# Kernel tuning notes

Hardware: AMD Instinct MI355X
Metric: run time of the kernel (lower is better)

Reference implementation:

```python
import jax, jax.numpy as jnp
import numpy as np

DIM = 768
NUM_HEADS = 12
POLY_DEG = 3
GRID = (24, 24)
BATCH = 16


def _make_powers():
    H, W = GRID
    ii, jj = np.meshgrid(np.arange(H), np.arange(W), indexing='ij')
    coords = np.stack([ii.ravel(), jj.ravel()], axis=-1).astype(np.float32)  # [HW, 2]
    dists = np.abs(coords[:, None, :] - coords[None, :, :]).sum(-1)  # L1 cdist [HW, HW]
    powers = np.stack([dists ** i for i in range(POLY_DEG + 1)], axis=0)  # [deg+1, HW, HW]
    return jnp.asarray(powers, dtype=jnp.float32)


def setup_inputs() -> dict:
    key = jax.random.key(0)
    ks = jax.random.split(key, 5)
    N = GRID[0] * GRID[1] + 1  # 577
    x = jax.random.normal(ks[0], (BATCH, N, DIM), dtype=jnp.float32)
    # nn.Linear weights stored as [in, out] for direct matmul; qkv_bias=False
    W_qkv = jax.random.normal(ks[1], (DIM, 3 * DIM), dtype=jnp.float32) * (DIM ** -0.5)
    W_proj = jax.random.normal(ks[2], (DIM, DIM), dtype=jnp.float32) * (DIM ** -0.5)
    b_proj = jnp.zeros((DIM,), dtype=jnp.float32)
    # small scale keeps polynomial bias (distances up to 46, cubed) numerically sane
    poly_coeffs = jax.random.normal(ks[3], (NUM_HEADS, POLY_DEG + 1), dtype=jnp.float32) * 0.01
    powers = _make_powers()
    return {"x": x, "W_qkv": W_qkv, "W_proj": W_proj, "b_proj": b_proj,
            "poly_coeffs": poly_coeffs, "powers": powers}


def reference(x, W_qkv, W_proj, b_proj, poly_coeffs, powers):
    B, N, C = x.shape
    h = NUM_HEADS
    d = C // h
    scale = d ** -0.5
    qkv = (x @ W_qkv).reshape(B, N, 3, h, d)
    qkv = jnp.transpose(qkv, (2, 0, 3, 1, 4))  # [3, B, h, N, d]
    q, k, v = qkv[0], qkv[1], qkv[2]
    # polynomial relative-position bias, padded with zeros for CLS row/col
    rpe = jnp.einsum('hd,dxy->hxy', poly_coeffs, powers)  # [h, HW, HW]
    rpe = jnp.pad(rpe, ((0, 0), (1, 0), (1, 0)))  # [h, N, N]
    attn = scale * jnp.einsum('bhnd,bhmd->bhnm', q, k) + rpe[None]
    attn = jax.nn.softmax(attn, axis=-1)
    out = jnp.einsum('bhnm,bhmd->bhnd', attn, v)
    out = jnp.transpose(out, (0, 2, 1, 3)).reshape(B, N, C)
    return out @ W_proj + b_proj
```

## Files before the change

kernel.cpp:

```cpp
#include <hip/hip_runtime.h>


using u16 = unsigned short;
using u32 = unsigned int;

typedef __bf16 bf16x8 __attribute__((ext_vector_type(8)));
typedef float f32x4 __attribute__((ext_vector_type(4)));

__device__ inline u16 f2bf(float f) {
    u32 u = __builtin_bit_cast(u32, f);
    u32 r = u + 0x7fffu + ((u >> 16) & 1u);
    return (u16)(r >> 16);
}
__device__ inline float bf2f(u16 x) {
    return __builtin_bit_cast(float, (u32)x << 16);
}

__device__ inline f32x4 mfma16(bf16x8 a, bf16x8 b, f32x4 c) {
    return __builtin_amdgcn_mfma_f32_16x16x32_bf16(a, b, c, 0, 0, 0);
}

__device__ inline float fexp2(float x) { return __builtin_amdgcn_exp2f(x); }

__device__ inline float dpp_max16(float v) {
    int x;
    x = __builtin_amdgcn_update_dpp(0, __builtin_bit_cast(int, v), 0xB1, 0xF, 0xF, true);
    v = fmaxf(v, __builtin_bit_cast(float, x));
    x = __builtin_amdgcn_update_dpp(0, __builtin_bit_cast(int, v), 0x4E, 0xF, 0xF, true);
    v = fmaxf(v, __builtin_bit_cast(float, x));
    x = __builtin_amdgcn_update_dpp(0, __builtin_bit_cast(int, v), 0x124, 0xF, 0xF, true);
    v = fmaxf(v, __builtin_bit_cast(float, x));
    x = __builtin_amdgcn_update_dpp(0, __builtin_bit_cast(int, v), 0x128, 0xF, 0xF, true);
    v = fmaxf(v, __builtin_bit_cast(float, x));
    return v;
}
__device__ inline float dpp_sum16(float v) {
    int x;
    x = __builtin_amdgcn_update_dpp(0, __builtin_bit_cast(int, v), 0xB1, 0xF, 0xF, true);
    v += __builtin_bit_cast(float, x);
    x = __builtin_amdgcn_update_dpp(0, __builtin_bit_cast(int, v), 0x4E, 0xF, 0xF, true);
    v += __builtin_bit_cast(float, x);
    x = __builtin_amdgcn_update_dpp(0, __builtin_bit_cast(int, v), 0x124, 0xF, 0xF, true);
    v += __builtin_bit_cast(float, x);
    x = __builtin_amdgcn_update_dpp(0, __builtin_bit_cast(int, v), 0x128, 0xF, 0xF, true);
    v += __builtin_bit_cast(float, x);
    return v;
}

#define GLOAD_LDS16(g, l)                                                          \
    __builtin_amdgcn_global_load_lds((const __attribute__((address_space(1))) u32*)(g), \
                                     (__attribute__((address_space(3))) u32*)(l), 16, 0, 0)

#define BAR()    asm volatile("s_barrier" ::: "memory")
#define WAITV4() asm volatile("s_waitcnt vmcnt(4)" ::: "memory")
#define WAITV0() asm volatile("s_waitcnt vmcnt(0)" ::: "memory")

__global__ void k_prep(const float* __restrict__ x, const float* __restrict__ Wq,
                       const float* __restrict__ Wp, u16* __restrict__ xb,
                       u16* __restrict__ wqkv, u16* __restrict__ wprj) {
    const int tid0 = blockIdx.x * blockDim.x + threadIdx.x;
    const int stride = gridDim.x * blockDim.x;
    const int n4 = 9232 * 768 / 4;
    for (int i = tid0; i < n4; i += stride) {
        float4 v = ((const float4*)x)[i];
        ushort4 o;
        o.x = f2bf(v.x); o.y = f2bf(v.y); o.z = f2bf(v.z); o.w = f2bf(v.w);
        ((ushort4*)xb)[i] = o;
    }
    for (int i = tid0; i < 768 * 2304; i += stride) {
        int r = i / 2304, c = i - r * 2304;
        wqkv[(size_t)c * 768 + r] = f2bf(Wq[i]);
    }
    for (int i = tid0; i < 768 * 768; i += stride) {
        int r = i / 768, c = i - r * 768;
        wprj[(size_t)c * 768 + r] = f2bf(Wp[i]);
    }
}

__device__ inline void stageAB(const u16* __restrict__ Ag, const u16* __restrict__ Bg,
                               u16* La, u16* Lb, int t, int w) {
#pragma unroll
    for (int c = 0; c < 2; ++c) {
        const int p = c * 256 + t;
        const int row = p >> 2, ch = p & 3;
        const int src = row * 768 + ((ch ^ ((row >> 1) & 3)) * 8);
        GLOAD_LDS16(Ag + src, La + (size_t)(c * 256 + w * 64) * 8);
        GLOAD_LDS16(Bg + src, Lb + (size_t)(c * 256 + w * 64) * 8);
    }
}
__device__ inline bf16x8 ldfrag32(const u16* base, int row, int slot) {
    return *(const bf16x8*)(base + row * 32 + ((slot ^ ((row >> 1) & 3)) * 8));
}

template <int MODE>
__launch_bounds__(256, 3)
__global__ void k_gemm(const u16* __restrict__ A, const u16* __restrict__ Bw,
                       u16* __restrict__ q_out, u16* __restrict__ k_out,
                       u16* __restrict__ v_out,
                       float* __restrict__ f_out, const float* __restrict__ bias) {
    constexpr int NT = 24;
    constexpr int M = 9232;
    const int mbase = blockIdx.y * 128;
    const int nbase = blockIdx.x * 128;
    __shared__ alignas(16) u16 lds[3][2][128 * 32];
    const int t = threadIdx.x;
    const int lane = t & 63, w = t >> 6;
    const int lr = lane & 15, lg = lane >> 4;
    const int wrow = (w >> 1) * 64, wcol = (w & 1) * 64;
    const u16* Ag = A + (size_t)mbase * 768;
    const u16* Bg = Bw + (size_t)nbase * 768;
    f32x4 acc[4][4] = {};

    stageAB(Ag, Bg, &lds[0][0][0], &lds[0][1][0], t, w);
    stageAB(Ag + 32, Bg + 32, &lds[1][0][0], &lds[1][1][0], t, w);
    WAITV4();
    BAR();

    for (int kt = 0; kt < NT; ++kt) {
        const int cb = kt % 3;
        const u16* Ab = &lds[cb][0][0];
        const u16* Bb = &lds[cb][1][0];
        const bool m2 = (kt + 2) < NT;
        if (m2) {
            const int nb = (kt + 2) % 3;
            stageAB(Ag + (kt + 2) * 32, Bg + (kt + 2) * 32,
                    &lds[nb][0][0], &lds[nb][1][0], t, w);
        }
        bf16x8 af[4], bv[4];
#pragma unroll
        for (int i = 0; i < 4; ++i)
            af[i] = ldfrag32(Ab, wrow + i * 16 + lr, lg);
#pragma unroll
        for (int j = 0; j < 4; ++j)
            bv[j] = ldfrag32(Bb, wcol + j * 16 + lr, lg);
        __builtin_amdgcn_s_setprio(1);
#pragma unroll
        for (int i = 0; i < 4; ++i)
#pragma unroll
            for (int j = 0; j < 4; ++j)
                acc[i][j] = mfma16(af[i], bv[j], acc[i][j]);
        __builtin_amdgcn_s_setprio(0);
        if (kt + 1 < NT) {
            if (m2) { WAITV4(); } else { WAITV0(); }
            BAR();
        }
    }

#pragma unroll
    for (int i = 0; i < 4; ++i) {
#pragma unroll
        for (int j = 0; j < 4; ++j) {
            const int col = nbase + wcol + j * 16 + lr;
#pragma unroll
            for (int r = 0; r < 4; ++r) {
                const int row = mbase + wrow + i * 16 + 4 * lg + r;
                if (row < M) {
                    if (MODE == 0) {
                        const int bb = row / 577;
                        const int nn = row - bb * 577;
                        const int tt = col / 768;
                        const int rem = col - tt * 768;
                        const int hh = rem >> 6, dd = rem & 63;
                        const size_t bh = (size_t)bb * 12 + hh;
                        const u16 val = f2bf(acc[i][j][r]);
                        if (tt == 0)      q_out[(bh * 640 + nn) * 64 + dd] = val;
                        else if (tt == 1) k_out[(bh * 640 + nn) * 64 + dd] = val;
                        else              v_out[(bh * 64 + dd) * 640 + nn] = val;
                    } else {
                        f_out[(size_t)row * 768 + col] = acc[i][j][r] + bias[col];
                    }
                }
            }
        }
    }
}

__launch_bounds__(256, 3)
__global__ void k_attn(const u16* __restrict__ Qg, const u16* __restrict__ Kg,
                       const u16* __restrict__ Vtg, const float* __restrict__ coef,
                       u16* __restrict__ Og) {
    const int bh = blockIdx.x;
    const int qt = blockIdx.y;
    const int b = bh / 12, h = bh - b * 12;
    const int t = threadIdx.x;
    const int lane = t & 63, w = t >> 6;
    const int lr = lane & 15, lg = lane >> 4;
    __shared__ alignas(16) u16 Kl[2][4096];
    __shared__ alignas(16) u16 Vl[2][4096];
    __shared__ alignas(16) u16 Plds[4][16 * 72];
    __shared__ float lut[256];

    {
        const float l2e = 1.4426950408889634f;
        const float c0 = coef[h * 4 + 0] * l2e, c1 = coef[h * 4 + 1] * l2e,
                    c2 = coef[h * 4 + 2] * l2e, c3 = coef[h * 4 + 3] * l2e;
        const float d = (float)t;
        lut[t] = (t <= 46) ? (((c3 * d + c2) * d + c1) * d + c0) : 0.f;
    }

    const int qrow0 = qt * 64 + w * 16;
    const u16* qp = Qg + ((size_t)bh * 640 + qrow0 + lr) * 64;
    const bf16x8 qa0 = *(const bf16x8*)(qp + lg * 8);
    const bf16x8 qa1 = *(const bf16x8*)(qp + 32 + lg * 8);

    float gi[4], gj[4];
#pragma unroll
    for (int r = 0; r < 4; ++r) {
        const int n = qrow0 + 4 * lg + r;
        if (n == 0) { gi[r] = 100.f; gj[r] = 0.f; }
        else {
            const int nm1 = n - 1;
            const int qi = nm1 / 24;
            gi[r] = (float)qi;
            gj[r] = (float)(nm1 - qi * 24);
        }
    }

    float M[4], L[4];
#pragma unroll
    for (int r = 0; r < 4; ++r) { M[r] = -3e38f; L[r] = 0.f; }
    f32x4 acco[4] = {};
    const float scale2 = 0.125f * 1.4426950408889634f;
    const int ch0 = ((lg ^ (lr & 7))) * 8;

    const u16* Ksb = Kg + (size_t)bh * 640 * 64;
    const u16* Vsb = Vtg + (size_t)bh * 64 * 640;
    const int pr0 = t >> 3, pc0 = t & 7;
    const int pr1 = (256 + t) >> 3, pc1 = (256 + t) & 7;
    const int kd0 = pr0 * 64 + ((pc0 ^ (pr0 & 7)) * 8);
    const int kd1 = pr1 * 64 + ((pc1 ^ (pr1 & 7)) * 8);

    {
        uint4 k0 = *(const uint4*)(Ksb + pr0 * 64 + pc0 * 8);
        uint4 k1 = *(const uint4*)(Ksb + pr1 * 64 + pc1 * 8);
        uint4 v0 = *(const uint4*)(Vsb + (size_t)pr0 * 640 + pc0 * 8);
        uint4 v1 = *(const uint4*)(Vsb + (size_t)pr1 * 640 + pc1 * 8);
        *(uint4*)(&Kl[0][kd0]) = k0;
        *(uint4*)(&Kl[0][kd1]) = k1;
        *(uint4*)(&Vl[0][kd0]) = v0;
        *(uint4*)(&Vl[0][kd1]) = v1;
    }
    __syncthreads();
    int cur = 0;

    for (int kt = 0; kt < 10; ++kt) {
        const bool full = (kt < 9);
        uint4 nk0, nk1, nv0, nv1;
        if (full) {
            const u16* Ks = Ksb + (size_t)(kt + 1) * 64 * 64;
            const u16* Vs = Vsb + (size_t)(kt + 1) * 64;
            nk0 = *(const uint4*)(Ks + pr0 * 64 + pc0 * 8);
            nk1 = *(const uint4*)(Ks + pr1 * 64 + pc1 * 8);
            nv0 = *(const uint4*)(Vs + (size_t)pr0 * 640 + pc0 * 8);
            nv1 = *(const uint4*)(Vs + (size_t)pr1 * 640 + pc1 * 8);
        }
        const u16* Kc = &Kl[cur][0];
        const u16* Vc = &Vl[cur][0];

        f32x4 sac[4];
#pragma unroll
        for (int cb = 0; cb < 4; ++cb) {
            if (full || cb == 0) {
                const int row = cb * 16 + lr;
                const bf16x8 kb0 = *(const bf16x8*)(Kc + row * 64 + ch0);
                const bf16x8 kb1 = *(const bf16x8*)(Kc + row * 64 + (ch0 ^ 32));
                f32x4 z = {};
                z = mfma16(qa0, kb0, z);
                sac[cb] = mfma16(qa1, kb1, z);
            }
        }

        float s[4][4], tm[4];
#pragma unroll
        for (int r = 0; r < 4; ++r) tm[r] = -3e38f;
#pragma unroll
        for (int cb = 0; cb < 4; ++cb) {
            if (full || cb == 0) {
                const int m = kt * 64 + cb * 16 + lr;
                float ci, cj;
                if (m == 0) { ci = 200.f; cj = 0.f; }
                else {
                    const int mm1 = m - 1;
                    const int pi = mm1 / 24;
                    ci = (float)pi;
                    cj = (float)(mm1 - pi * 24);
                }
#pragma unroll
                for (int r = 0; r < 4; ++r) {
                    const float df = fabsf(gi[r] - ci) + fabsf(gj[r] - cj);
                    const int idx = (int)df;
                    float v = fmaf(sac[cb][r], scale2, lut[idx]);
                    if (!full) v = (lr == 0) ? v : -1e30f;
                    s[cb][r] = v;
                    tm[r] = fmaxf(tm[r], v);
                }
            } else {
#pragma unroll
                for (int r = 0; r < 4; ++r) s[cb][r] = -1e30f;
            }
        }
#pragma unroll
        for (int r = 0; r < 4; ++r) tm[r] = dpp_max16(tm[r]);

        float over = tm[0] - M[0];
        over = fmaxf(over, tm[1] - M[1]);
        over = fmaxf(over, tm[2] - M[2]);
        over = fmaxf(over, tm[3] - M[3]);
        if (__any(over > 11.5f)) {
#pragma unroll
            for (int r = 0; r < 4; ++r) {
                const float Mn = fmaxf(M[r], tm[r]);
                const float a = fexp2(M[r] - Mn);
                L[r] *= a;
                acco[0][r] *= a; acco[1][r] *= a;
                acco[2][r] *= a; acco[3][r] *= a;
                M[r] = Mn;
            }
        }

        u16* pw = &Plds[w][0];
#pragma unroll
        for (int cb = 0; cb < 4; ++cb)
#pragma unroll
            for (int r = 0; r < 4; ++r) {
                const float p = fexp2(s[cb][r] - M[r]);
                L[r] += p;
                pw[(4 * lg + r) * 72 + cb * 16 + lr] = f2bf(p);
            }
        const bf16x8 pa0 = *(const bf16x8*)(pw + lr * 72 + lg * 8);
        const bf16x8 pa1 = *(const bf16x8*)(pw + lr * 72 + 32 + lg * 8);
#pragma unroll
        for (int f = 0; f < 4; ++f) {
            const int vrow = f * 16 + lr;
            const bf16x8 vb0 = *(const bf16x8*)(Vc + vrow * 64 + ch0);
            acco[f] = mfma16(pa0, vb0, acco[f]);
            if (full) {
                const bf16x8 vb1 = *(const bf16x8*)(Vc + vrow * 64 + (ch0 ^ 32));
                acco[f] = mfma16(pa1, vb1, acco[f]);
            }
        }

        if (full) {
            __syncthreads();
            *(uint4*)(&Kl[cur ^ 1][kd0]) = nk0;
            *(uint4*)(&Kl[cur ^ 1][kd1]) = nk1;
            *(uint4*)(&Vl[cur ^ 1][kd0]) = nv0;
            *(uint4*)(&Vl[cur ^ 1][kd1]) = nv1;
            __syncthreads();
            cur ^= 1;
        }
    }

    float inv[4];
#pragma unroll
    for (int r = 0; r < 4; ++r) inv[r] = __builtin_amdgcn_rcpf(dpp_sum16(L[r]));
#pragma unroll
    for (int f = 0; f < 4; ++f)
#pragma unroll
        for (int r = 0; r < 4; ++r) {
            const int n = qrow0 + 4 * lg + r;
            Og[((size_t)b * 577 + n) * 768 + h * 64 + f * 16 + lr] =
                f2bf(acco[f][r] * inv[r]);
        }
}

__launch_bounds__(256)
__global__ void k_attn_last(const u16* __restrict__ Qg, const u16* __restrict__ Kg,
                            const u16* __restrict__ Vtg, const float* __restrict__ coef,
                            u16* __restrict__ Og) {
    const int bh = blockIdx.x;
    const int b = bh / 12, h = bh - b * 12;
    const int t = threadIdx.x;
    const int lane = t & 63, w = t >> 6;
    __shared__ float qs[64];
    __shared__ float ps[640];
    __shared__ float red[4];
    __shared__ float opart[4][64];
    const float l2e = 1.4426950408889634f;
    const float c0 = coef[h * 4 + 0] * l2e, c1 = coef[h * 4 + 1] * l2e,
                c2 = coef[h * 4 + 2] * l2e, c3 = coef[h * 4 + 3] * l2e;
    const float scale2 = 0.125f * l2e;

    if (t < 64) qs[t] = bf2f(Qg[((size_t)bh * 640 + 576) * 64 + t]);
    __syncthreads();

    float sv[3];
#pragma unroll
    for (int u = 0; u < 3; ++u) {
        const int k = t + u * 256;
        float s = -3e38f;
        if (k < 577) {
            const u16* kp = Kg + ((size_t)bh * 640 + k) * 64;
            float acc = 0.f;
            for (int j = 0; j < 64; ++j) acc += qs[j] * bf2f(kp[j]);
            float rv = 0.f;
            if (k >= 1) {
                const int km1 = k - 1;
                const int ki = km1 / 24;
                const float d = fabsf(23.f - (float)ki) + fabsf(23.f - (float)(km1 - ki * 24));
                rv = ((c3 * d + c2) * d + c1) * d + c0;
            }
            s = fmaf(acc, scale2, rv);
        }
        sv[u] = s;
    }
    float v = fmaxf(fmaxf(sv[0], sv[1]), sv[2]);
    v = fmaxf(v, __shfl_xor(v, 1));  v = fmaxf(v, __shfl_xor(v, 2));
    v = fmaxf(v, __shfl_xor(v, 4));  v = fmaxf(v, __shfl_xor(v, 8));
    v = fmaxf(v, __shfl_xor(v, 16)); v = fmaxf(v, __shfl_xor(v, 32));
    if (lane == 0) red[w] = v;
    __syncthreads();
    const float Mx = fmaxf(fmaxf(red[0], red[1]), fmaxf(red[2], red[3]));

    float lsum = 0.f;
#pragma unroll
    for (int u = 0; u < 3; ++u) {
        const int k = t + u * 256;
        const float p = (k < 577) ? fexp2(sv[u] - Mx) : 0.f;
        if (k < 640) ps[k] = p;
        lsum += p;
    }
    lsum += __shfl_xor(lsum, 1);  lsum += __shfl_xor(lsum, 2);
    lsum += __shfl_xor(lsum, 4);  lsum += __shfl_xor(lsum, 8);
    lsum += __shfl_xor(lsum, 16); lsum += __shfl_xor(lsum, 32);
    __syncthreads();
    if (lane == 0) red[w] = lsum;
    __syncthreads();
    const float Lx = red[0] + red[1] + red[2] + red[3];

    const int d = t & 63, qd = t >> 6;
    const u16* vp = Vtg + ((size_t)bh * 64 + d) * 640;
    float o = 0.f;
    for (int k = qd * 160; k < qd * 160 + 160; ++k) o += ps[k] * bf2f(vp[k]);
    opart[qd][d] = o;
    __syncthreads();
    if (t < 64) {
        const float oo = (opart[0][t] + opart[1][t] + opart[2][t] + opart[3][t]) / Lx;
        Og[((size_t)b * 577 + 576) * 768 + h * 64 + t] = f2bf(oo);
    }
}

extern "C" void kernel_launch(void* const* d_in, const int* in_sizes, int n_in,
                              void* d_out, int out_size, void* d_ws, size_t ws_size,
                              hipStream_t stream) {
    const float* x      = (const float*)d_in[0];
    const float* W_qkv  = (const float*)d_in[1];
    const float* W_proj = (const float*)d_in[2];
    const float* b_proj = (const float*)d_in[3];
    const float* coef   = (const float*)d_in[4];
    float* out = (float*)d_out;
    char* ws = (char*)d_ws;

    u16* xb   = (u16*)(ws + 0);
    u16* Og   = (u16*)(ws + 14180352);
    u16* wqkv = (u16*)(ws + 28360704);
    u16* wprj = (u16*)(ws + 31899648);
    u16* Qg   = (u16*)(ws + 33079296);
    u16* Kg   = (u16*)(ws + 48807936);
    u16* Vtg  = (u16*)(ws + 64536576);

    hipMemsetAsync(Vtg, 0, 15728640, stream);

    k_prep<<<2048, 256, 0, stream>>>(x, W_qkv, W_proj, xb, wqkv, wprj);

    k_gemm<0><<<dim3(18, 73), 256, 0, stream>>>(xb, wqkv, Qg, Kg, Vtg,
                                                nullptr, nullptr);
    k_attn<<<dim3(192, 9), 256, 0, stream>>>(Qg, Kg, Vtg, coef, Og);
    k_attn_last<<<192, 256, 0, stream>>>(Qg, Kg, Vtg, coef, Og);
    k_gemm<1><<<dim3(6, 73), 256, 0, stream>>>(Og, wprj, nullptr, nullptr,
                                               nullptr, out, b_proj);
}
```

Before: 195.2 us.

## Precompute RPE bias table in prep and remap GEMM blocks across XCDs

Replaces the per-block LDS polynomial LUT and in-loop grid-distance computation in attention with a precomputed, log2e-scaled bias table written by the prep kernel and loaded from global memory. GEMM launches become 1D with an XCD-aware block remap to improve L2 locality, and attention grid axes are swapped so query tiles of the same head run adjacently. This trades ALU work for an extra large table write and read traffic, and the workspace layout is reshuffled with Og aliasing xb.

```diff
diff --git a/kernel.cpp b/kernel.cpp
--- a/kernel.cpp
+++ b/kernel.cpp
@@ -21,6 +21,12 @@
 }
 
 __device__ inline float fexp2(float x) { return __builtin_amdgcn_exp2f(x); }
+
+__device__ inline int xcd_remap(int bid, int nwg) {
+    const int q = nwg >> 3, r = nwg & 7;
+    const int xcd = bid & 7, idx = bid >> 3;
+    return (xcd < r ? xcd * (q + 1) : r * (q + 1) + (xcd - r) * q) + idx;
+}
 
 __device__ inline float dpp_max16(float v) {
     int x;
@@ -56,8 +62,9 @@
 #define WAITV0() asm volatile("s_waitcnt vmcnt(0)" ::: "memory")
 
 __global__ void k_prep(const float* __restrict__ x, const float* __restrict__ Wq,
-                       const float* __restrict__ Wp, u16* __restrict__ xb,
-                       u16* __restrict__ wqkv, u16* __restrict__ wprj) {
+                       const float* __restrict__ Wp, const float* __restrict__ coef,
+                       u16* __restrict__ xb, u16* __restrict__ wqkv,
+                       u16* __restrict__ wprj, float* __restrict__ rpe2) {
     const int tid0 = blockIdx.x * blockDim.x + threadIdx.x;
     const int stride = gridDim.x * blockDim.x;
     const int n4 = 9232 * 768 / 4;
@@ -75,6 +82,22 @@
         int r = i / 768, c = i - r * 768;
         wprj[(size_t)c * 768 + r] = f2bf(Wp[i]);
     }
+    const float l2e = 1.4426950408889634f;
+    for (int i = tid0; i < 12 * 576 * 640; i += stride) {
+        const int h = i / (576 * 640);
+        const int rem = i - h * (576 * 640);
+        const int n = rem / 640, m = rem - (rem / 640) * 640;
+        float v = 0.f;
+        if (n >= 1 && m >= 1 && m <= 576) {
+            const int qi = (n - 1) / 24, qj = (n - 1) - qi * 24;
+            const int ki = (m - 1) / 24, kj = (m - 1) - ki * 24;
+            const float d = (float)(abs(qi - ki) + abs(qj - kj));
+            const float c0 = coef[h * 4 + 0], c1 = coef[h * 4 + 1],
+                        c2 = coef[h * 4 + 2], c3 = coef[h * 4 + 3];
+            v = (((c3 * d + c2) * d + c1) * d + c0) * l2e;
+        }
+        rpe2[i] = v;
+    }
 }
 
 __device__ inline void stageAB(const u16* __restrict__ Ag, const u16* __restrict__ Bg,
@@ -92,7 +115,7 @@
     return *(const bf16x8*)(base + row * 32 + ((slot ^ ((row >> 1) & 3)) * 8));
 }
 
-template <int MODE>
+template <int MODE, int NB>
 __launch_bounds__(256, 3)
 __global__ void k_gemm(const u16* __restrict__ A, const u16* __restrict__ Bw,
                        u16* __restrict__ q_out, u16* __restrict__ k_out,
@@ -100,8 +123,9 @@
                        float* __restrict__ f_out, const float* __restrict__ bias) {
     constexpr int NT = 24;
     constexpr int M = 9232;
-    const int mbase = blockIdx.y * 128;
-    const int nbase = blockIdx.x * 128;
+    const int wgid = xcd_remap(blockIdx.x, gridDim.x);
+    const int mbase = (wgid / NB) * 128;
+    const int nbase = (wgid - (wgid / NB) * NB) * 128;
     __shared__ alignas(16) u16 lds[3][2][128 * 32];
     const int t = threadIdx.x;
     const int lane = t & 63, w = t >> 6;
@@ -177,10 +201,10 @@
 
 __launch_bounds__(256, 3)
 __global__ void k_attn(const u16* __restrict__ Qg, const u16* __restrict__ Kg,
-                       const u16* __restrict__ Vtg, const float* __restrict__ coef,
+                       const u16* __restrict__ Vtg, const float* __restrict__ rpe2,
                        u16* __restrict__ Og) {
-    const int bh = blockIdx.x;
-    const int qt = blockIdx.y;
+    const int qt = blockIdx.x;
+    const int bh = blockIdx.y;
     const int b = bh / 12, h = bh - b * 12;
     const int t = threadIdx.x;
     const int lane = t & 63, w = t >> 6;
@@ -188,33 +212,16 @@
     __shared__ alignas(16) u16 Kl[2][4096];
     __shared__ alignas(16) u16 Vl[2][4096];
     __shared__ alignas(16) u16 Plds[4][16 * 72];
-    __shared__ float lut[256];
-
-    {
-        const float l2e = 1.4426950408889634f;
-        const float c0 = coef[h * 4 + 0] * l2e, c1 = coef[h * 4 + 1] * l2e,
-                    c2 = coef[h * 4 + 2] * l2e, c3 = coef[h * 4 + 3] * l2e;
-        const float d = (float)t;
-        lut[t] = (t <= 46) ? (((c3 * d + c2) * d + c1) * d + c0) : 0.f;
-    }
 
     const int qrow0 = qt * 64 + w * 16;
     const u16* qp = Qg + ((size_t)bh * 640 + qrow0 + lr) * 64;
     const bf16x8 qa0 = *(const bf16x8*)(qp + lg * 8);
     const bf16x8 qa1 = *(const bf16x8*)(qp + 32 + lg * 8);
 
-    float gi[4], gj[4];
-#pragma unroll
-    for (int r = 0; r < 4; ++r) {
-        const int n = qrow0 + 4 * lg + r;
-        if (n == 0) { gi[r] = 100.f; gj[r] = 0.f; }
-        else {
-            const int nm1 = n - 1;
-            const int qi = nm1 / 24;
-            gi[r] = (float)qi;
-            gj[r] = (float)(nm1 - qi * 24);
-        }
-    }
+    const float* rb[4];
+#pragma unroll
+    for (int r = 0; r < 4; ++r)
+        rb[r] = rpe2 + ((size_t)h * 576 + (qrow0 + 4 * lg + r)) * 640;
 
     float M[4], L[4];
 #pragma unroll
@@ -254,6 +261,14 @@
             nv0 = *(const uint4*)(Vs + (size_t)pr0 * 640 + pc0 * 8);
             nv1 = *(const uint4*)(Vs + (size_t)pr1 * 640 + pc1 * 8);
         }
+        const int mo = kt * 64 + lr;
+        float rp[4][4];
+#pragma unroll
+        for (int cb = 0; cb < 4; ++cb)
+#pragma unroll
+            for (int r = 0; r < 4; ++r)
+                rp[cb][r] = rb[r][mo + cb * 16];
+
         const u16* Kc = &Kl[cur][0];
         const u16* Vc = &Vl[cur][0];
 
@@ -276,20 +291,9 @@
 #pragma unroll
         for (int cb = 0; cb < 4; ++cb) {
             if (full || cb == 0) {
-                const int m = kt * 64 + cb * 16 + lr;
-                float ci, cj;
-                if (m == 0) { ci = 200.f; cj = 0.f; }
-                else {
-                    const int mm1 = m - 1;
-                    const int pi = mm1 / 24;
-                    ci = (float)pi;
-                    cj = (float)(mm1 - pi * 24);
-                }
 #pragma unroll
                 for (int r = 0; r < 4; ++r) {
-                    const float df = fabsf(gi[r] - ci) + fabsf(gj[r] - cj);
-                    const int idx = (int)df;
-                    float v = fmaf(sac[cb][r], scale2, lut[idx]);
+                    float v = fmaf(sac[cb][r], scale2, rp[cb][r]);
                     if (!full) v = (lr == 0) ? v : -1e30f;
                     s[cb][r] = v;
                     tm[r] = fmaxf(tm[r], v);
@@ -451,22 +455,23 @@
     float* out = (float*)d_out;
     char* ws = (char*)d_ws;
 
-    u16* xb   = (u16*)(ws + 0);
-    u16* Og   = (u16*)(ws + 14180352);
-    u16* wqkv = (u16*)(ws + 28360704);
-    u16* wprj = (u16*)(ws + 31899648);
-    u16* Qg   = (u16*)(ws + 33079296);
-    u16* Kg   = (u16*)(ws + 48807936);
-    u16* Vtg  = (u16*)(ws + 64536576);
+    u16*   xb   = (u16*)(ws + 0);
+    u16*   Og   = (u16*)(ws + 0);
+    u16*   wqkv = (u16*)(ws + 14180352);
+    u16*   wprj = (u16*)(ws + 17719296);
+    float* rpe2 = (float*)(ws + 18898944);
+    u16*   Qg   = (u16*)(ws + 36593664);
+    u16*   Kg   = (u16*)(ws + 52322304);
+    u16*   Vtg  = (u16*)(ws + 68050944);
 
     hipMemsetAsync(Vtg, 0, 15728640, stream);
 
-    k_prep<<<2048, 256, 0, stream>>>(x, W_qkv, W_proj, xb, wqkv, wprj);
-
-    k_gemm<0><<<dim3(18, 73), 256, 0, stream>>>(xb, wqkv, Qg, Kg, Vtg,
-                                                nullptr, nullptr);
-    k_attn<<<dim3(192, 9), 256, 0, stream>>>(Qg, Kg, Vtg, coef, Og);
+    k_prep<<<2048, 256, 0, stream>>>(x, W_qkv, W_proj, coef, xb, wqkv, wprj, rpe2);
+
+    k_gemm<0, 18><<<18 * 73, 256, 0, stream>>>(xb, wqkv, Qg, Kg, Vtg,
+                                               nullptr, nullptr);
+    k_attn<<<dim3(9, 192), 256, 0, stream>>>(Qg, Kg, Vtg, rpe2, Og);
     k_attn_last<<<192, 256, 0, stream>>>(Qg, Kg, Vtg, coef, Og);
-    k_gemm<1><<<dim3(6, 73), 256, 0, stream>>>(Og, wprj, nullptr, nullptr,
-                                               nullptr, out, b_proj);
-}
+    k_gemm<1, 6><<<6 * 73, 256, 0, stream>>>(Og, wprj, nullptr, nullptr,
+                                             nullptr, out, b_proj);
+}
```

Result: slower. 207.0 us (+6.1%).

## Widen QKV GEMM tiles, add XCD-aware block remap, drop V memset

Applied to the files above, without the earlier changes.

The QKV projection GEMM now uses 128x256 tiles (NJ=8) at 2 blocks/CU, so each A tile is reused across twice as many output columns. A 1D grid is remapped so consecutive tiles land on the same XCD and share L2. The attention grid is transposed so query tiles of the same head are adjacent. The workspace is re-laid out so Og aliases xb, and the memset of the padded V buffer is removed. That removal relies on attention never reading or using the padded V columns; if it does, uninitialised memory could leak into the output.

```diff
diff --git a/kernel.cpp b/kernel.cpp
--- a/kernel.cpp
+++ b/kernel.cpp
@@ -21,6 +21,12 @@
 }
 
 __device__ inline float fexp2(float x) { return __builtin_amdgcn_exp2f(x); }
+
+__device__ inline int xcd_remap(int bid, int nwg) {
+    const int q = nwg >> 3, r = nwg & 7;
+    const int xcd = bid & 7, idx = bid >> 3;
+    return (xcd < r ? xcd * (q + 1) : r * (q + 1) + (xcd - r) * q) + idx;
+}
 
 __device__ inline float dpp_max16(float v) {
     int x;
@@ -52,6 +58,7 @@
                                      (__attribute__((address_space(3))) u32*)(l), 16, 0, 0)
 
 #define BAR()    asm volatile("s_barrier" ::: "memory")
+#define WAITV6() asm volatile("s_waitcnt vmcnt(6)" ::: "memory")
 #define WAITV4() asm volatile("s_waitcnt vmcnt(4)" ::: "memory")
 #define WAITV0() asm volatile("s_waitcnt vmcnt(0)" ::: "memory")
 
@@ -77,71 +84,76 @@
     }
 }
 
+template <int NJ>
 __device__ inline void stageAB(const u16* __restrict__ Ag, const u16* __restrict__ Bg,
-                               u16* La, u16* Lb, int t, int w) {
+                               u16* L, int t) {
 #pragma unroll
     for (int c = 0; c < 2; ++c) {
         const int p = c * 256 + t;
         const int row = p >> 2, ch = p & 3;
-        const int src = row * 768 + ((ch ^ ((row >> 1) & 3)) * 8);
-        GLOAD_LDS16(Ag + src, La + (size_t)(c * 256 + w * 64) * 8);
-        GLOAD_LDS16(Bg + src, Lb + (size_t)(c * 256 + w * 64) * 8);
+        GLOAD_LDS16(Ag + row * 768 + ((ch ^ ((row >> 1) & 3)) * 8), L + p * 8);
+    }
+#pragma unroll
+    for (int c = 0; c < NJ / 2; ++c) {
+        const int p = c * 256 + t;
+        const int row = p >> 2, ch = p & 3;
+        GLOAD_LDS16(Bg + row * 768 + ((ch ^ ((row >> 1) & 3)) * 8),
+                    L + 4096 + p * 8);
     }
 }
 __device__ inline bf16x8 ldfrag32(const u16* base, int row, int slot) {
     return *(const bf16x8*)(base + row * 32 + ((slot ^ ((row >> 1) & 3)) * 8));
 }
 
-template <int MODE>
-__launch_bounds__(256, 3)
+template <int MODE, int NB, int NJ>
+__launch_bounds__(256, NJ == 8 ? 2 : 3)
 __global__ void k_gemm(const u16* __restrict__ A, const u16* __restrict__ Bw,
                        u16* __restrict__ q_out, u16* __restrict__ k_out,
                        u16* __restrict__ v_out,
                        float* __restrict__ f_out, const float* __restrict__ bias) {
     constexpr int NT = 24;
     constexpr int M = 9232;
-    const int mbase = blockIdx.y * 128;
-    const int nbase = blockIdx.x * 128;
-    __shared__ alignas(16) u16 lds[3][2][128 * 32];
+    constexpr int BN = NJ * 32;
+    const int wgid = xcd_remap(blockIdx.x, gridDim.x);
+    const int mbase = (wgid / NB) * 128;
+    const int nbase = (wgid - (wgid / NB) * NB) * BN;
+    __shared__ alignas(16) u16 lds[3][4096 + NJ * 1024];
     const int t = threadIdx.x;
     const int lane = t & 63, w = t >> 6;
     const int lr = lane & 15, lg = lane >> 4;
-    const int wrow = (w >> 1) * 64, wcol = (w & 1) * 64;
+    const int wrow = (w >> 1) * 64, wcol = (w & 1) * (NJ * 16);
     const u16* Ag = A + (size_t)mbase * 768;
     const u16* Bg = Bw + (size_t)nbase * 768;
-    f32x4 acc[4][4] = {};
-
-    stageAB(Ag, Bg, &lds[0][0][0], &lds[0][1][0], t, w);
-    stageAB(Ag + 32, Bg + 32, &lds[1][0][0], &lds[1][1][0], t, w);
-    WAITV4();
+    f32x4 acc[4][NJ] = {};
+
+    stageAB<NJ>(Ag, Bg, &lds[0][0], t);
+    stageAB<NJ>(Ag + 32, Bg + 32, &lds[1][0], t);
+    if (NJ == 8) { WAITV6(); } else { WAITV4(); }
     BAR();
 
     for (int kt = 0; kt < NT; ++kt) {
-        const int cb = kt % 3;
-        const u16* Ab = &lds[cb][0][0];
-        const u16* Bb = &lds[cb][1][0];
+        const u16* Lc = &lds[kt % 3][0];
         const bool m2 = (kt + 2) < NT;
-        if (m2) {
-            const int nb = (kt + 2) % 3;
-            stageAB(Ag + (kt + 2) * 32, Bg + (kt + 2) * 32,
-                    &lds[nb][0][0], &lds[nb][1][0], t, w);
-        }
-        bf16x8 af[4], bv[4];
+        if (m2)
+            stageAB<NJ>(Ag + (kt + 2) * 32, Bg + (kt + 2) * 32,
+                        &lds[(kt + 2) % 3][0], t);
+        bf16x8 af[4], bv[NJ];
 #pragma unroll
         for (int i = 0; i < 4; ++i)
-            af[i] = ldfrag32(Ab, wrow + i * 16 + lr, lg);
-#pragma unroll
-        for (int j = 0; j < 4; ++j)
-            bv[j] = ldfrag32(Bb, wcol + j * 16 + lr, lg);
+            af[i] = ldfrag32(Lc, wrow + i * 16 + lr, lg);
+#pragma unroll
+        for (int j = 0; j < NJ; ++j)
+            bv[j] = ldfrag32(Lc + 4096, wcol + j * 16 + lr, lg);
         __builtin_amdgcn_s_setprio(1);
 #pragma unroll
         for (int i = 0; i < 4; ++i)
 #pragma unroll
-            for (int j = 0; j < 4; ++j)
+            for (int j = 0; j < NJ; ++j)
                 acc[i][j] = mfma16(af[i], bv[j], acc[i][j]);
         __builtin_amdgcn_s_setprio(0);
         if (kt + 1 < NT) {
-            if (m2) { WAITV4(); } else { WAITV0(); }
+            if (m2) { if (NJ == 8) { WAITV6(); } else { WAITV4(); } }
+            else    { WAITV0(); }
             BAR();
         }
     }
@@ -149,7 +161,7 @@
 #pragma unroll
     for (int i = 0; i < 4; ++i) {
 #pragma unroll
-        for (int j = 0; j < 4; ++j) {
+        for (int j = 0; j < NJ; ++j) {
             const int col = nbase + wcol + j * 16 + lr;
 #pragma unroll
             for (int r = 0; r < 4; ++r) {
@@ -179,8 +191,8 @@
 __global__ void k_attn(const u16* __restrict__ Qg, const u16* __restrict__ Kg,
                        const u16* __restrict__ Vtg, const float* __restrict__ coef,
                        u16* __restrict__ Og) {
-    const int bh = blockIdx.x;
-    const int qt = blockIdx.y;
+    const int qt = blockIdx.x;
+    const int bh = blockIdx.y;
     const int b = bh / 12, h = bh - b * 12;
     const int t = threadIdx.x;
     const int lane = t & 63, w = t >> 6;
@@ -452,21 +464,19 @@
     char* ws = (char*)d_ws;
 
     u16* xb   = (u16*)(ws + 0);
-    u16* Og   = (u16*)(ws + 14180352);
-    u16* wqkv = (u16*)(ws + 28360704);
-    u16* wprj = (u16*)(ws + 31899648);
-    u16* Qg   = (u16*)(ws + 33079296);
-    u16* Kg   = (u16*)(ws + 48807936);
-    u16* Vtg  = (u16*)(ws + 64536576);
-
-    hipMemsetAsync(Vtg, 0, 15728640, stream);
+    u16* Og   = (u16*)(ws + 0);
+    u16* wqkv = (u16*)(ws + 14180352);
+    u16* wprj = (u16*)(ws + 17719296);
+    u16* Qg   = (u16*)(ws + 18898944);
+    u16* Kg   = (u16*)(ws + 34627584);
+    u16* Vtg  = (u16*)(ws + 50356224);
 
     k_prep<<<2048, 256, 0, stream>>>(x, W_qkv, W_proj, xb, wqkv, wprj);
 
-    k_gemm<0><<<dim3(18, 73), 256, 0, stream>>>(xb, wqkv, Qg, Kg, Vtg,
+    k_gemm<0, 9, 8><<<9 * 73, 256, 0, stream>>>(xb, wqkv, Qg, Kg, Vtg,
                                                 nullptr, nullptr);
-    k_attn<<<dim3(192, 9), 256, 0, stream>>>(Qg, Kg, Vtg, coef, Og);
+    k_attn<<<dim3(9, 192), 256, 0, stream>>>(Qg, Kg, Vtg, coef, Og);
     k_attn_last<<<192, 256, 0, stream>>>(Qg, Kg, Vtg, coef, Og);
-    k_gemm<1><<<dim3(6, 73), 256, 0, stream>>>(Og, wprj, nullptr, nullptr,
-                                               nullptr, out, b_proj);
-}
+    k_gemm<1, 6, 4><<<6 * 73, 256, 0, stream>>>(Og, wprj, nullptr, nullptr,
+                                                nullptr, out, b_proj);
+}
```

Result: faster. 184.5 us (-5.5%).
